# Kernel tuning notes

Measured on AMD Instinct MI355X. Metric: run time of the kernel, lower is better.

The kernel has to match this reference:

```python
import jax, jax.numpy as jnp
import numpy as np

N_NODES = 100000
N_EDGES = 1600000
HIDDEN = 48
LAYERS = 4
ALPHA = 0.1
THETA = 0.5


def setup_inputs() -> dict:
    key = jax.random.key(0)
    ks = jax.random.split(key, 6)
    x = jax.random.normal(ks[0], (N_NODES, 3), dtype=jnp.float32)
    edge_index = jax.random.randint(ks[1], (2, N_EDGES), 0, N_NODES, dtype=jnp.int32)
    W0 = jax.random.normal(ks[2], (3, HIDDEN), dtype=jnp.float32) * 0.3
    b0 = jnp.zeros((HIDDEN,), dtype=jnp.float32)
    convW = jax.random.normal(ks[3], (LAYERS, HIDDEN, HIDDEN), dtype=jnp.float32) * (1.0 / np.sqrt(HIDDEN))
    W1 = jax.random.normal(ks[4], (HIDDEN, HIDDEN), dtype=jnp.float32) * (1.0 / np.sqrt(HIDDEN))
    b1 = jnp.zeros((HIDDEN,), dtype=jnp.float32)
    return {"x": x, "edge_index": edge_index, "W0": W0, "b0": b0,
            "convW": convW, "W1": W1, "b1": b1}


def reference(x, edge_index, W0, b0, convW, W1, b1):
    # lin0 + relu; x0 is the initial residual (dropout=0 / eval mode -> identity)
    h = jax.nn.relu(x @ W0 + b0)
    x0 = h
    src, dst = edge_index[0], edge_index[1]
    n = h.shape[0]
    for l in range(LAYERS):
        # sparse propagation: A @ h via gather + segment_sum (unit edge weights, normalize=False)
        agg = jax.ops.segment_sum(h[src], dst, num_segments=n)
        beta = float(np.log(THETA / (l + 1) + 1.0))
        # GCNII shared-weights branch: t = (1-alpha)*Ah + alpha*x0; out = (1-beta)*t + beta*(t @ W)
        t = (1.0 - ALPHA) * agg + ALPHA * x0
        h = jax.nn.relu((1.0 - beta) * t + beta * (t @ convW[l]))
    out = h @ W1 + b1
    return jax.nn.log_softmax(out, axis=-1)
```

## Files before the change

kernel.cpp:

```cpp
#include <hip/hip_runtime.h>
#include <math.h>

#define N_NODES 100000
#define N_EDGES 1600000
#define HID 48
#define HPAD 64
#define ALPHA 0.1f

#define LBLK 6250
#define NPW 4

typedef unsigned short u16;
typedef unsigned int u32;

__device__ __forceinline__ float bf_lo(u32 u) { return __uint_as_float(u << 16); }
__device__ __forceinline__ float bf_hi(u32 u) { return __uint_as_float(u & 0xffff0000u); }
__device__ __forceinline__ u16 f2bf(float f) {
    u32 b = __float_as_uint(f);
    b += 0x7fff + ((b >> 16) & 1);
    return (u16)(b >> 16);
}
__device__ __forceinline__ u32 pack2(float a, float b) {
    return (u32)f2bf(a) | ((u32)f2bf(b) << 16);
}

#define RLANE(x, l) __int_as_float(__builtin_amdgcn_readlane(__float_as_int(x), (l)))

__global__ __launch_bounds__(256) void lin0_k(const float* __restrict__ x, const float* __restrict__ W0,
                                              const float* __restrict__ b0, u16* __restrict__ h0) {
    int t = blockIdx.x * 256 + threadIdx.x;
    if (t >= N_NODES * 6) return;
    int node = t / 6, oct = t % 6;
    float xv0 = x[node * 3 + 0], xv1 = x[node * 3 + 1], xv2 = x[node * 3 + 2];
    float v[8];
#pragma unroll
    for (int j = 0; j < 8; j++) {
        int f = oct * 8 + j;
        float s = b0[f] + xv0 * W0[0 * HID + f] + xv1 * W0[1 * HID + f] + xv2 * W0[2 * HID + f];
        v[j] = s > 0.f ? s : 0.f;
    }
    uint4 p;
    p.x = pack2(v[0], v[1]); p.y = pack2(v[2], v[3]);
    p.z = pack2(v[4], v[5]); p.w = pack2(v[6], v[7]);
    *(uint4*)(h0 + (size_t)node * HPAD + oct * 8) = p;
}

__global__ __launch_bounds__(256) void count_k(const int* __restrict__ dst, int* __restrict__ deg,
                                               int* __restrict__ rank) {
    int e = blockIdx.x * 256 + threadIdx.x;
    if (e < N_EDGES) rank[e] = atomicAdd(&deg[dst[e]], 1);
}

__global__ __launch_bounds__(256) void scan1_k(const int* __restrict__ deg, int* __restrict__ rowptr,
                                               int* __restrict__ partial) {
    __shared__ int sums[256];
    int tid = threadIdx.x;
    int base = blockIdx.x * 2048 + tid * 8;
    int v[8]; int s = 0;
#pragma unroll
    for (int j = 0; j < 8; j++) { int idx = base + j; v[j] = (idx < N_NODES) ? deg[idx] : 0; s += v[j]; }
    sums[tid] = s; __syncthreads();
    for (int off = 1; off < 256; off <<= 1) {
        int t = (tid >= off) ? sums[tid - off] : 0;
        __syncthreads();
        sums[tid] += t;
        __syncthreads();
    }
    if (tid == 255) partial[blockIdx.x] = sums[255];
    int run = (tid > 0) ? sums[tid - 1] : 0;
#pragma unroll
    for (int j = 0; j < 8; j++) { int idx = base + j; if (idx < N_NODES) rowptr[idx] = run; run += v[j]; }
}

__global__ void scan2_k(int* __restrict__ partial, int* __restrict__ rowptr, int nblk) {
    int lane = threadIdx.x & 63;
    int v = (lane < nblk) ? partial[lane] : 0;
    for (int off = 1; off < 64; off <<= 1) {
        int t = __shfl_up(v, off);
        if (lane >= off) v += t;
    }
    int excl = __shfl_up(v, 1);
    if (lane == 0) excl = 0;
    if (lane < nblk) partial[lane] = excl;
    if (lane == 63) rowptr[N_NODES] = v;
}

__global__ __launch_bounds__(256) void scan3_k(int* __restrict__ rowptr, const int* __restrict__ partial) {
    int tid = threadIdx.x;
    int base = blockIdx.x * 2048 + tid * 8;
    int add = partial[blockIdx.x];
#pragma unroll
    for (int j = 0; j < 8; j++) {
        int idx = base + j;
        if (idx < N_NODES) rowptr[idx] += add;
    }
}

__global__ __launch_bounds__(256) void bucket_k(const int* __restrict__ src, const int* __restrict__ dst,
                                                const int* __restrict__ rank, const int* __restrict__ rowptr,
                                                int* __restrict__ ssrc) {
    int e = blockIdx.x * 256 + threadIdx.x;
    if (e < N_EDGES) {
        int d = dst[e];
        ssrc[rowptr[d] + rank[e]] = src[e];
    }
}

struct PF { int e0, e1; uint4 wA, wB, wC; };

__device__ __forceinline__ PF pf_load(const u16* __restrict__ h_in, const int* __restrict__ rowptr,
                                      const int* __restrict__ ssrc, int node, int slot, int cc) {
    PF p;
    p.e0 = rowptr[node];
    p.e1 = rowptr[node + 1];
    int es = p.e0 < N_EDGES ? p.e0 : N_EDGES - 1;
    int iA = p.e0 + slot, iB = p.e0 + 8 + slot, iC = p.e0 + 16 + slot;
    int sA = ssrc[iA < p.e1 ? iA : es];
    int sB = ssrc[iB < p.e1 ? iB : es];
    int sC = ssrc[iC < p.e1 ? iC : es];
    p.wA = *(const uint4*)(h_in + ((size_t)sA << 6) + cc * 8);
    p.wB = *(const uint4*)(h_in + ((size_t)sB << 6) + cc * 8);
    p.wC = *(const uint4*)(h_in + ((size_t)sC << 6) + cc * 8);
    return p;
}

__device__ __forceinline__ void acc8(float& a0, float& a1, float& a2, float& a3,
                                     float& a4, float& a5, float& a6, float& a7, const uint4& w) {
    a0 += bf_lo(w.x); a1 += bf_hi(w.x);
    a2 += bf_lo(w.y); a3 += bf_hi(w.y);
    a4 += bf_lo(w.z); a5 += bf_hi(w.z);
    a6 += bf_lo(w.w); a7 += bf_hi(w.w);
}

__device__ __forceinline__ void process_node(const PF& p, int node, int slot, int cc, int lane,
                                             const float (&wreg)[48],
                                             const u16* __restrict__ h_in, const u16* __restrict__ x0,
                                             const int* __restrict__ ssrc, u16* __restrict__ h_out) {
    const uint4 xv = *(const uint4*)(x0 + ((size_t)node << 6) + cc * 8);
    float a0 = 0.f, a1 = 0.f, a2 = 0.f, a3 = 0.f, a4 = 0.f, a5 = 0.f, a6 = 0.f, a7 = 0.f;
    int e0 = p.e0, e1 = p.e1;
    if (e0 + slot < e1)      acc8(a0, a1, a2, a3, a4, a5, a6, a7, p.wA);
    if (e0 + 8 + slot < e1)  acc8(a0, a1, a2, a3, a4, a5, a6, a7, p.wB);
    if (e0 + 16 + slot < e1) acc8(a0, a1, a2, a3, a4, a5, a6, a7, p.wC);
    for (int e = e0 + 24; e < e1; e += 8) {
        int idx = e + slot;
        int s = ssrc[idx < e1 ? idx : e];
        const uint4 w = *(const uint4*)(h_in + ((size_t)s << 6) + cc * 8);
        if (idx < e1) acc8(a0, a1, a2, a3, a4, a5, a6, a7, w);
    }
#pragma unroll
    for (int off = 8; off <= 32; off <<= 1) {
        a0 += __shfl_xor(a0, off); a1 += __shfl_xor(a1, off);
        a2 += __shfl_xor(a2, off); a3 += __shfl_xor(a3, off);
        a4 += __shfl_xor(a4, off); a5 += __shfl_xor(a5, off);
        a6 += __shfl_xor(a6, off); a7 += __shfl_xor(a7, off);
    }
    a0 = (1.f - ALPHA) * a0 + ALPHA * bf_lo(xv.x);
    a1 = (1.f - ALPHA) * a1 + ALPHA * bf_hi(xv.x);
    a2 = (1.f - ALPHA) * a2 + ALPHA * bf_lo(xv.y);
    a3 = (1.f - ALPHA) * a3 + ALPHA * bf_hi(xv.y);
    a4 = (1.f - ALPHA) * a4 + ALPHA * bf_lo(xv.z);
    a5 = (1.f - ALPHA) * a5 + ALPHA * bf_hi(xv.z);
    a6 = (1.f - ALPHA) * a6 + ALPHA * bf_lo(xv.w);
    a7 = (1.f - ALPHA) * a7 + ALPHA * bf_hi(xv.w);
    float p0 = 0.f, p1 = 0.f, p2 = 0.f, p3 = 0.f;
#pragma unroll
    for (int c = 0; c < 6; ++c) {
        p0 = fmaf(RLANE(a0, c), wreg[c * 8 + 0], p0);
        p1 = fmaf(RLANE(a1, c), wreg[c * 8 + 1], p1);
        p2 = fmaf(RLANE(a2, c), wreg[c * 8 + 2], p2);
        p3 = fmaf(RLANE(a3, c), wreg[c * 8 + 3], p3);
        p0 = fmaf(RLANE(a4, c), wreg[c * 8 + 4], p0);
        p1 = fmaf(RLANE(a5, c), wreg[c * 8 + 5], p1);
        p2 = fmaf(RLANE(a6, c), wreg[c * 8 + 6], p2);
        p3 = fmaf(RLANE(a7, c), wreg[c * 8 + 7], p3);
    }
    float o = (p0 + p1) + (p2 + p3);
    if (lane < 48) h_out[((size_t)node << 6) + lane] = f2bf(o > 0.f ? o : 0.f);
}

__global__ __launch_bounds__(256) void layer_k(const u16* __restrict__ h_in, const u16* __restrict__ x0,
                                               const int* __restrict__ rowptr, const int* __restrict__ ssrc,
                                               const float* __restrict__ W, float beta,
                                               u16* __restrict__ h_out) {
    __shared__ float sM[2304];
    int tid = threadIdx.x, lane = tid & 63;
    for (int i = tid; i < 2304; i += 256) {
        int r = i / 48, c = i - r * 48;
        float v = beta * W[i];
        if (r == c) v += 1.f - beta;
        sM[i] = v;
    }
    __syncthreads();
    int f = lane < 48 ? lane : 0;
    float wreg[48];
#pragma unroll
    for (int r = 0; r < 48; ++r) wreg[r] = sM[r * 48 + f];

    int chunk = lane & 7;
    int slot  = lane >> 3;
    int cc = chunk < 6 ? chunk : 0;
    int wid = __builtin_amdgcn_readfirstlane(blockIdx.x * 4 + (tid >> 6));
    int base = wid * NPW;

    PF pA = pf_load(h_in, rowptr, ssrc, base + 0, slot, cc);
    PF pB = pf_load(h_in, rowptr, ssrc, base + 1, slot, cc);
    process_node(pA, base + 0, slot, cc, lane, wreg, h_in, x0, ssrc, h_out);
    PF pC = pf_load(h_in, rowptr, ssrc, base + 2, slot, cc);
    process_node(pB, base + 1, slot, cc, lane, wreg, h_in, x0, ssrc, h_out);
    PF pD = pf_load(h_in, rowptr, ssrc, base + 3, slot, cc);
    process_node(pC, base + 2, slot, cc, lane, wreg, h_in, x0, ssrc, h_out);
    process_node(pD, base + 3, slot, cc, lane, wreg, h_in, x0, ssrc, h_out);
}

__global__ __launch_bounds__(256) void final_k(const u16* __restrict__ h, const float* __restrict__ W1,
                                               const float* __restrict__ b1, float* __restrict__ out) {
    __shared__ float sW[2304];
    int tid = threadIdx.x, lane = tid & 63;
    for (int i = tid; i < 2304; i += 256) sW[i] = W1[i];
    __syncthreads();
    int f = lane < 48 ? lane : 0;
    float wreg[48];
#pragma unroll
    for (int r = 0; r < 48; ++r) wreg[r] = sW[r * 48 + f];
    float bv = b1[f];
    int chunk = lane & 7;
    int cc = chunk < 6 ? chunk : 0;
    int wid = blockIdx.x * 4 + (tid >> 6);

    for (int i = 0; i < NPW; ++i) {
        int node = wid * NPW + i;
        if (node >= N_NODES) break;
        const uint4 hv = *(const uint4*)(h + ((size_t)node << 6) + cc * 8);
        float a0 = bf_lo(hv.x), a1 = bf_hi(hv.x), a2 = bf_lo(hv.y), a3 = bf_hi(hv.y);
        float a4 = bf_lo(hv.z), a5 = bf_hi(hv.z), a6 = bf_lo(hv.w), a7 = bf_hi(hv.w);
        float p0 = bv, p1 = 0.f, p2 = 0.f, p3 = 0.f;
#pragma unroll
        for (int c = 0; c < 6; ++c) {
            p0 = fmaf(RLANE(a0, c), wreg[c * 8 + 0], p0);
            p1 = fmaf(RLANE(a1, c), wreg[c * 8 + 1], p1);
            p2 = fmaf(RLANE(a2, c), wreg[c * 8 + 2], p2);
            p3 = fmaf(RLANE(a3, c), wreg[c * 8 + 3], p3);
            p0 = fmaf(RLANE(a4, c), wreg[c * 8 + 4], p0);
            p1 = fmaf(RLANE(a5, c), wreg[c * 8 + 5], p1);
            p2 = fmaf(RLANE(a6, c), wreg[c * 8 + 6], p2);
            p3 = fmaf(RLANE(a7, c), wreg[c * 8 + 7], p3);
        }
        float v = (lane < 48) ? (p0 + p1) + (p2 + p3) : -INFINITY;
        float m = v;
        for (int off = 32; off >= 1; off >>= 1) m = fmaxf(m, __shfl_xor(m, off));
        float ex = (lane < 48) ? expf(v - m) : 0.f;
        float sum = ex;
        for (int off = 32; off >= 1; off >>= 1) sum += __shfl_xor(sum, off);
        if (lane < 48) out[(size_t)node * 48 + lane] = v - m - logf(sum);
    }
}

extern "C" void kernel_launch(void* const* d_in, const int* in_sizes, int n_in,
                              void* d_out, int out_size, void* d_ws, size_t ws_size,
                              hipStream_t stream) {
    const float* x     = (const float*)d_in[0];
    const int*   ei    = (const int*)d_in[1];
    const float* W0    = (const float*)d_in[2];
    const float* b0    = (const float*)d_in[3];
    const float* convW = (const float*)d_in[4];
    const float* W1    = (const float*)d_in[5];
    const float* b1    = (const float*)d_in[6];
    float* out = (float*)d_out;
    const int* src = ei;
    const int* dst = ei + N_EDGES;

    char* ws = (char*)d_ws;
    size_t off = 0;
    u16* h0 = (u16*)(ws + off); off += (size_t)N_NODES * HPAD * 2;
    u16* hA = (u16*)(ws + off); off += (size_t)N_NODES * HPAD * 2;
    u16* hB = (u16*)(ws + off); off += (size_t)N_NODES * HPAD * 2;
    int* rank = (int*)hA;
    int* ssrc = (int*)(ws + off);   off += (size_t)N_EDGES * 4;
    int* rowptr = (int*)(ws + off); off += (size_t)(N_NODES + 1) * 4;
    off = (off + 255) & ~(size_t)255;
    int* deg = (int*)(ws + off);    off += (size_t)N_NODES * 4;
    off = (off + 255) & ~(size_t)255;
    int* partial = (int*)(ws + off); off += 64 * 4;

    hipMemsetAsync(deg, 0, (size_t)N_NODES * 4, stream);

    lin0_k<<<(N_NODES * 6 + 255) / 256, 256, 0, stream>>>(x, W0, b0, h0);
    count_k<<<6250, 256, 0, stream>>>(dst, deg, rank);
    scan1_k<<<49, 256, 0, stream>>>(deg, rowptr, partial);
    scan2_k<<<1, 64, 0, stream>>>(partial, rowptr, 49);
    scan3_k<<<49, 256, 0, stream>>>(rowptr, partial);
    bucket_k<<<6250, 256, 0, stream>>>(src, dst, rank, rowptr, ssrc);

    const float betas[4] = { logf(1.5f), logf(1.25f), logf(7.f / 6.f), logf(1.125f) };

    layer_k<<<LBLK, 256, 0, stream>>>(h0, h0, rowptr, ssrc, convW + 0 * 2304, betas[0], hB);
    layer_k<<<LBLK, 256, 0, stream>>>(hB, h0, rowptr, ssrc, convW + 1 * 2304, betas[1], hA);
    layer_k<<<LBLK, 256, 0, stream>>>(hA, h0, rowptr, ssrc, convW + 2 * 2304, betas[2], hB);
    layer_k<<<LBLK, 256, 0, stream>>>(hB, h0, rowptr, ssrc, convW + 3 * 2304, betas[3], hA);
    final_k<<<LBLK, 256, 0, stream>>>(hA, W1, b1, out);
}
```

Measured before the change: 445.6 us.

## Fuse lin0 with edge counting, deepen layer prefetch, nontemporal bucket stores

```diff
diff --git a/kernel.cpp b/kernel.cpp
--- a/kernel.cpp
+++ b/kernel.cpp
@@ -7,8 +7,13 @@
 #define HPAD 64
 #define ALPHA 0.1f
 
-#define LBLK 6250
-#define NPW 4
+#define LBLK 3125
+#define NPW 8
+#define FBLK 6250
+#define FNPW 4
+
+#define CNT_BLK 3125
+#define LIN0_BLK 2344
 
 typedef unsigned short u16;
 typedef unsigned int u32;
@@ -26,29 +31,34 @@
 
 #define RLANE(x, l) __int_as_float(__builtin_amdgcn_readlane(__float_as_int(x), (l)))
 
-__global__ __launch_bounds__(256) void lin0_k(const float* __restrict__ x, const float* __restrict__ W0,
-                                              const float* __restrict__ b0, u16* __restrict__ h0) {
-    int t = blockIdx.x * 256 + threadIdx.x;
-    if (t >= N_NODES * 6) return;
-    int node = t / 6, oct = t % 6;
-    float xv0 = x[node * 3 + 0], xv1 = x[node * 3 + 1], xv2 = x[node * 3 + 2];
-    float v[8];
-#pragma unroll
-    for (int j = 0; j < 8; j++) {
-        int f = oct * 8 + j;
-        float s = b0[f] + xv0 * W0[0 * HID + f] + xv1 * W0[1 * HID + f] + xv2 * W0[2 * HID + f];
-        v[j] = s > 0.f ? s : 0.f;
-    }
-    uint4 p;
-    p.x = pack2(v[0], v[1]); p.y = pack2(v[2], v[3]);
-    p.z = pack2(v[4], v[5]); p.w = pack2(v[6], v[7]);
-    *(uint4*)(h0 + (size_t)node * HPAD + oct * 8) = p;
-}
-
-__global__ __launch_bounds__(256) void count_k(const int* __restrict__ dst, int* __restrict__ deg,
-                                               int* __restrict__ rank) {
-    int e = blockIdx.x * 256 + threadIdx.x;
-    if (e < N_EDGES) rank[e] = atomicAdd(&deg[dst[e]], 1);
+__global__ __launch_bounds__(256) void cl_k(const int* __restrict__ dst, int* __restrict__ deg,
+                                            int* __restrict__ rank,
+                                            const float* __restrict__ x, const float* __restrict__ W0,
+                                            const float* __restrict__ b0, u16* __restrict__ h0) {
+    int b = blockIdx.x;
+    if (b < CNT_BLK) {
+        int e = (b * 256 + threadIdx.x) * 2;
+        int2 d2 = *(const int2*)(dst + e);
+        int r0 = atomicAdd(&deg[d2.x], 1);
+        int r1 = atomicAdd(&deg[d2.y], 1);
+        *(int2*)(rank + e) = make_int2(r0, r1);
+    } else {
+        int t = (b - CNT_BLK) * 256 + threadIdx.x;
+        if (t >= N_NODES * 6) return;
+        int node = t / 6, oct = t % 6;
+        float xv0 = x[node * 3 + 0], xv1 = x[node * 3 + 1], xv2 = x[node * 3 + 2];
+        float v[8];
+#pragma unroll
+        for (int j = 0; j < 8; j++) {
+            int f = oct * 8 + j;
+            float s = b0[f] + xv0 * W0[0 * HID + f] + xv1 * W0[1 * HID + f] + xv2 * W0[2 * HID + f];
+            v[j] = s > 0.f ? s : 0.f;
+        }
+        uint4 p;
+        p.x = pack2(v[0], v[1]); p.y = pack2(v[2], v[3]);
+        p.z = pack2(v[4], v[5]); p.w = pack2(v[6], v[7]);
+        *(uint4*)(h0 + (size_t)node * HPAD + oct * 8) = p;
+    }
 }
 
 __global__ __launch_bounds__(256) void scan1_k(const int* __restrict__ deg, int* __restrict__ rowptr,
@@ -102,7 +112,8 @@
     int e = blockIdx.x * 256 + threadIdx.x;
     if (e < N_EDGES) {
         int d = dst[e];
-        ssrc[rowptr[d] + rank[e]] = src[e];
+        int s = src[e];
+        __builtin_nontemporal_store(s, ssrc + rowptr[d] + rank[e]);
     }
 }
 
@@ -203,14 +214,22 @@
     int wid = __builtin_amdgcn_readfirstlane(blockIdx.x * 4 + (tid >> 6));
     int base = wid * NPW;
 
-    PF pA = pf_load(h_in, rowptr, ssrc, base + 0, slot, cc);
-    PF pB = pf_load(h_in, rowptr, ssrc, base + 1, slot, cc);
-    process_node(pA, base + 0, slot, cc, lane, wreg, h_in, x0, ssrc, h_out);
-    PF pC = pf_load(h_in, rowptr, ssrc, base + 2, slot, cc);
-    process_node(pB, base + 1, slot, cc, lane, wreg, h_in, x0, ssrc, h_out);
-    PF pD = pf_load(h_in, rowptr, ssrc, base + 3, slot, cc);
-    process_node(pC, base + 2, slot, cc, lane, wreg, h_in, x0, ssrc, h_out);
-    process_node(pD, base + 3, slot, cc, lane, wreg, h_in, x0, ssrc, h_out);
+    PF A = pf_load(h_in, rowptr, ssrc, base + 0, slot, cc);
+    PF B = pf_load(h_in, rowptr, ssrc, base + 1, slot, cc);
+    PF C = pf_load(h_in, rowptr, ssrc, base + 2, slot, cc);
+    process_node(A, base + 0, slot, cc, lane, wreg, h_in, x0, ssrc, h_out);
+    A = pf_load(h_in, rowptr, ssrc, base + 3, slot, cc);
+    process_node(B, base + 1, slot, cc, lane, wreg, h_in, x0, ssrc, h_out);
+    B = pf_load(h_in, rowptr, ssrc, base + 4, slot, cc);
+    process_node(C, base + 2, slot, cc, lane, wreg, h_in, x0, ssrc, h_out);
+    C = pf_load(h_in, rowptr, ssrc, base + 5, slot, cc);
+    process_node(A, base + 3, slot, cc, lane, wreg, h_in, x0, ssrc, h_out);
+    A = pf_load(h_in, rowptr, ssrc, base + 6, slot, cc);
+    process_node(B, base + 4, slot, cc, lane, wreg, h_in, x0, ssrc, h_out);
+    B = pf_load(h_in, rowptr, ssrc, base + 7, slot, cc);
+    process_node(C, base + 5, slot, cc, lane, wreg, h_in, x0, ssrc, h_out);
+    process_node(A, base + 6, slot, cc, lane, wreg, h_in, x0, ssrc, h_out);
+    process_node(B, base + 7, slot, cc, lane, wreg, h_in, x0, ssrc, h_out);
 }
 
 __global__ __launch_bounds__(256) void final_k(const u16* __restrict__ h, const float* __restrict__ W1,
@@ -228,8 +247,8 @@
     int cc = chunk < 6 ? chunk : 0;
     int wid = blockIdx.x * 4 + (tid >> 6);
 
-    for (int i = 0; i < NPW; ++i) {
-        int node = wid * NPW + i;
+    for (int i = 0; i < FNPW; ++i) {
+        int node = wid * FNPW + i;
         if (node >= N_NODES) break;
         const uint4 hv = *(const uint4*)(h + ((size_t)node << 6) + cc * 8);
         float a0 = bf_lo(hv.x), a1 = bf_hi(hv.x), a2 = bf_lo(hv.y), a3 = bf_hi(hv.y);
@@ -285,8 +304,7 @@
 
     hipMemsetAsync(deg, 0, (size_t)N_NODES * 4, stream);
 
-    lin0_k<<<(N_NODES * 6 + 255) / 256, 256, 0, stream>>>(x, W0, b0, h0);
-    count_k<<<6250, 256, 0, stream>>>(dst, deg, rank);
+    cl_k<<<CNT_BLK + LIN0_BLK, 256, 0, stream>>>(dst, deg, rank, x, W0, b0, h0);
     scan1_k<<<49, 256, 0, stream>>>(deg, rowptr, partial);
     scan2_k<<<1, 64, 0, stream>>>(partial, rowptr, 49);
     scan3_k<<<49, 256, 0, stream>>>(rowptr, partial);
@@ -298,5 +316,5 @@
     layer_k<<<LBLK, 256, 0, stream>>>(hB, h0, rowptr, ssrc, convW + 1 * 2304, betas[1], hA);
     layer_k<<<LBLK, 256, 0, stream>>>(hA, h0, rowptr, ssrc, convW + 2 * 2304, betas[2], hB);
     layer_k<<<LBLK, 256, 0, stream>>>(hB, h0, rowptr, ssrc, convW + 3 * 2304, betas[3], hA);
-    final_k<<<LBLK, 256, 0, stream>>>(hA, W1, b1, out);
-}
+    final_k<<<FBLK, 256, 0, stream>>>(hA, W1, b1, out);
+}
```

Measured after the change: 468.8 us. 5.2% more time.
